# Performance work log

Measured on AMD Instinct MI355X. Metric: run time of the kernel, lower is better.

Reference implementation:

```python
import jax, jax.numpy as jnp
import numpy as np


def setup_inputs() -> dict:
    key = jax.random.key(0)
    k1, k2, k3, k4 = jax.random.split(key, 4)
    B, T, C, H = 8, 2048, 1024, 64
    x = jax.random.normal(k1, (B, T, C), dtype=jnp.float32)
    Wq = jax.random.normal(k2, (C, H), dtype=jnp.float32) * (C ** -0.5)
    Wk = jax.random.normal(k3, (C, H), dtype=jnp.float32) * (C ** -0.5)
    Wv = jax.random.normal(k4, (C, H), dtype=jnp.float32) * (C ** -0.5)
    return {"x": x, "Wq": Wq, "Wk": Wk, "Wv": Wv}


def reference(x, Wq, Wk, Wv):
    # x: [B,T,C]; Wq/Wk/Wv: [C,H] (nn.Linear bias=False => x @ W)
    B, T, C = x.shape
    H = Wq.shape[-1]
    q = jnp.einsum('btc,ch->bth', x, Wq)
    k = jnp.einsum('btc,ch->bth', x, Wk)
    v = jnp.einsum('btc,ch->bth', x, Wv)
    scale = H ** -0.5
    att = jnp.einsum('bqh,bkh->bqk', q, k) * scale  # [B,T,T]
    causal = jnp.tril(jnp.ones((T, T), dtype=bool))
    att = jnp.where(causal, att, -jnp.inf)
    att = jax.nn.softmax(att, axis=-1)
    out = jnp.einsum('bqk,bkh->bqh', att, v)  # [B,T,H]
    return out
```

## Files before the change

### kernel.cpp

```cpp
#include <hip/hip_runtime.h>
#include <hip/hip_bf16.h>
#include <math.h>

#define BB 8
#define TT 2048
#define CC 1024
#define HH 64
#define BT (BB * TT)

typedef __attribute__((ext_vector_type(8))) short short8;
typedef __attribute__((ext_vector_type(4))) float floatx4;

static __device__ inline ushort f2bf(float f) {
    __hip_bfloat16 h = __float2bfloat16(f);
    return *reinterpret_cast<ushort*>(&h);
}
static __device__ inline unsigned int f2bf2(float lo, float hi) {
    __hip_bfloat162 h = __float22bfloat162_rn(make_float2(lo, hi));
    return *reinterpret_cast<unsigned int*>(&h);
}
static __device__ inline float bf2f(ushort u) {
    union { unsigned int i; float f; } c;
    c.i = ((unsigned int)u) << 16;
    return c.f;
}
static __device__ inline void gl_ldsf(const float* g, float* l) {
    __builtin_amdgcn_global_load_lds(
        (const __attribute__((address_space(1))) unsigned int*)g,
        (__attribute__((address_space(3))) unsigned int*)l,
        16, 0, 0);
}

__global__ __launch_bounds__(256) void wprep_kernel(
    const float* __restrict__ Wq, const float* __restrict__ Wk,
    const float* __restrict__ Wv, ushort* __restrict__ WbT)
{
    __shared__ float ws_[64 * 65];
    const int m  = blockIdx.x >> 4;
    const int kb = (blockIdx.x & 15) * 64;
    const float* W = (m == 0) ? Wq : (m == 1) ? Wk : Wv;
    const int t  = threadIdx.x;
    const int lr = t >> 4, lc = (t & 15) * 4;
    #pragma unroll
    for (int i = 0; i < 4; ++i) {
        const int row = lr + i * 16;
        float4 v = *(const float4*)&W[(size_t)(kb + row) * HH + lc];
        ws_[row * 65 + lc + 0] = v.x; ws_[row * 65 + lc + 1] = v.y;
        ws_[row * 65 + lc + 2] = v.z; ws_[row * 65 + lc + 3] = v.w;
    }
    __syncthreads();
    const int n = t & 63, kseg = t >> 6;
    union { ushort s[16]; uint4 q[2]; } u;
    #pragma unroll
    for (int j = 0; j < 16; ++j)
        u.s[j] = f2bf(ws_[(kseg * 16 + j) * 65 + n]);
    ushort* dst = &WbT[(size_t)(m * 64 + n) * 1024 + kb + kseg * 16];
    *(uint4*)&dst[0] = u.q[0];
    *(uint4*)&dst[8] = u.q[1];
}

__global__ __launch_bounds__(256) void qkv_kernel(
    const float* __restrict__ x, const ushort* __restrict__ WbT,
    ushort* __restrict__ qb, ushort* __restrict__ kbS, ushort* __restrict__ vS)
{
    __shared__ __align__(16) float Xs[4][2048];

    const int row0 = blockIdx.x * 32;
    const int t    = threadIdx.x;
    const int w    = t >> 6;
    const int lane = t & 63;
    const int l16  = lane & 15;
    const int quad = lane >> 4;
    const int ct0  = w * 3;

    const int d0 = lane & 1, d1 = (lane >> 1) & 1, d2 = (lane >> 2) & 1, d3 = (lane >> 3) & 1;
    const int quads = (d1 ^ d2 ^ d3) + 2 * (d2 ^ d3);
    const int hh    = d0 ^ d1 ^ d2 ^ d3;
    const int kof   = (w >> 1) * 32 + quads * 8 + hh * 4;
    const int rowA  = (w & 1) * 16 + ((lane >> 3) & 7);
    const float* srcA = &x[(size_t)(row0 + rowA) * CC + kof];
    const float* srcB = srcA + (size_t)8 * CC;

    int off[4][2];
    #pragma unroll
    for (int f = 0; f < 4; ++f) {
        const int Sr = f * 64 + l16 * 4 + quad;
        const int sw = (Sr & 7) << 4;
        off[f][0] = (Sr * 32) ^ sw;
        off[f][1] = (Sr * 32 + 16) ^ sw;
    }

    floatx4 acc[2][3];
    #pragma unroll
    for (int mt = 0; mt < 2; ++mt)
        #pragma unroll
        for (int c = 0; c < 3; ++c) acc[mt][c] = (floatx4){0.f, 0.f, 0.f, 0.f};

    #define STAGE(buf, itx) do {                                   \
        gl_ldsf(srcA + (itx) * 64, &Xs[buf][w * 512]);             \
        gl_ldsf(srcB + (itx) * 64, &Xs[buf][w * 512 + 256]);       \
    } while (0)

    STAGE(0, 0); STAGE(1, 1); STAGE(2, 2);
    asm volatile("" ::: "memory");

    short8 bW[2][2][3];
    #pragma unroll
    for (int s = 0; s < 2; ++s)
        #pragma unroll
        for (int p = 0; p < 2; ++p)
            #pragma unroll
            for (int c = 0; c < 3; ++c)
                bW[s][p][c] = *(const short8*)&WbT[(size_t)((ct0 + c) * 16 + l16) * 1024
                                                   + s * 64 + p * 32 + quad * 8];

    #pragma unroll
    for (int it = 0; it < 16; ++it) {
        if (it == 0)       asm volatile("s_waitcnt vmcnt(16)" ::: "memory");
        else if (it < 14)  asm volatile("s_waitcnt vmcnt(22)" ::: "memory");
        else if (it == 14) asm volatile("s_waitcnt vmcnt(20)" ::: "memory");
        else               asm volatile("s_waitcnt vmcnt(12)" ::: "memory");
        __builtin_amdgcn_s_barrier();

        if (it + 3 < 16) STAGE((it + 3) & 3, it + 3);
        asm volatile("" ::: "memory");

        const char* bufc = (const char*)&Xs[it & 3][0];
        short8 a[4];
        #pragma unroll
        for (int f = 0; f < 4; ++f) {
            float4 lo = *(const float4*)(bufc + off[f][0]);
            float4 hi = *(const float4*)(bufc + off[f][1]);
            union { unsigned int u[4]; short8 s; } cv;
            cv.u[0] = f2bf2(lo.x, lo.y); cv.u[1] = f2bf2(lo.z, lo.w);
            cv.u[2] = f2bf2(hi.x, hi.y); cv.u[3] = f2bf2(hi.z, hi.w);
            a[f] = cv.s;
        }

        __builtin_amdgcn_s_setprio(1);
        #pragma unroll
        for (int c = 0; c < 3; ++c) {
            acc[0][c] = __builtin_amdgcn_mfma_f32_16x16x32_bf16(a[0], bW[it & 1][0][c], acc[0][c], 0, 0, 0);
            acc[1][c] = __builtin_amdgcn_mfma_f32_16x16x32_bf16(a[1], bW[it & 1][0][c], acc[1][c], 0, 0, 0);
            acc[0][c] = __builtin_amdgcn_mfma_f32_16x16x32_bf16(a[2], bW[it & 1][1][c], acc[0][c], 0, 0, 0);
            acc[1][c] = __builtin_amdgcn_mfma_f32_16x16x32_bf16(a[3], bW[it & 1][1][c], acc[1][c], 0, 0, 0);
        }
        __builtin_amdgcn_s_setprio(0);

        if (it + 2 < 16) {
            const int kn = (it + 2) * 64;
            #pragma unroll
            for (int p = 0; p < 2; ++p)
                #pragma unroll
                for (int c = 0; c < 3; ++c)
                    bW[it & 1][p][c] = *(const short8*)&WbT[(size_t)((ct0 + c) * 16 + l16) * 1024
                                                            + kn + p * 32 + quad * 8];
        }
    }
    #undef STAGE

    const int half = (row0 >> 5) & 1;
    const size_t tile = (size_t)(row0 >> 6) * 4096;
    #pragma unroll
    for (int c = 0; c < 3; ++c) {
        const int ct    = ct0 + c;
        const int mtype = ct >> 2;
        const int n0    = (ct & 3) * 16;
        #pragma unroll
        for (int mt = 0; mt < 2; ++mt) {
            const int row = row0 + mt * 16 + quad * 4;
            if (mtype == 0) {
                #pragma unroll
                for (int reg = 0; reg < 4; ++reg)
                    qb[(size_t)(row + reg) * HH + n0 + l16] = f2bf(acc[mt][c][reg] * 0.125f);
            } else if (mtype == 1) {
                const int cP    = half * 2 + mt;
                const int pP    = (ct & 3) >> 1;
                const int quadP = ((ct & 3) * 2 + (l16 >> 3)) & 3;
                const int jP    = l16 & 7;
                const int ub    = (cP * 2 + pP) * 64 + quadP * 16;
                #pragma unroll
                for (int reg = 0; reg < 4; ++reg)
                    kbS[tile + (size_t)(ub + quad * 4 + reg) * 8 + jP] = f2bf(acc[mt][c][reg]);
            } else {
                const int cp2 = (ct & 3) * 2 + half;
                #pragma unroll
                for (int reg = 0; reg < 4; ++reg) {
                    const int rq    = quad * 4 + reg;
                    const int quadP = mt * 2 + (rq >> 3);
                    vS[tile + (size_t)(cp2 * 64 + quadP * 16 + l16) * 8 + (rq & 7)] = f2bf(acc[mt][c][reg]);
                }
            }
        }
    }
}

__global__ __launch_bounds__(256) void attn_kernel(
    const ushort* __restrict__ qb, const ushort* __restrict__ kbS,
    const ushort* __restrict__ vS, ushort* __restrict__ Opart,
    float* __restrict__ ml)
{
    __shared__ __align__(16) ushort P[4][16 * 72];

    const int t    = threadIdx.x;
    const int w    = t >> 6;
    const int lane = t & 63;
    const int l16  = lane & 15;
    const int quad = lane >> 4;

    const int b   = blockIdx.x & 7;
    const int idx = blockIdx.x >> 3;
    int qt, part, np;
    if (idx < 32)      { qt = 31 - (idx >> 2); part = idx & 3; np = 4; }
    else if (idx < 56) { const int u = idx - 32; const int g = u / 3;
                         qt = 23 - g; part = u - g * 3; np = 3; }
    else if (idx < 72) { const int u = idx - 56; qt = 15 - (u >> 1); part = u & 1; np = 2; }
    else               { qt = 7 - (idx - 72); part = 0; np = 1; }
    const int ntiles = qt + 1;
    const int ktb = (part * ntiles) / np;
    const int kte = ((part + 1) * ntiles) / np;

    const ushort* ktile0 = kbS + (size_t)(b * 32) * 4096;
    const ushort* vtile0 = vS  + (size_t)(b * 32) * 4096;

    short8 qf[2];
    {
        const ushort* qrow = qb + ((size_t)b * TT + qt * 64 + w * 16) * HH;
        qf[0] = *(const short8*)&qrow[l16 * HH + quad * 8];
        qf[1] = *(const short8*)&qrow[l16 * HH + 32 + quad * 8];
    }
    short8 ones;
    #pragma unroll
    for (int i = 0; i < 8; ++i) ones[i] = (short)0x3F80;

    floatx4 o[4], osum;
    #pragma unroll
    for (int c = 0; c < 4; ++c) o[c] = (floatx4){0.f, 0.f, 0.f, 0.f};
    osum = (floatx4){0.f, 0.f, 0.f, 0.f};

    ushort* Pw = &P[w][0];

    for (int kt = ktb; kt < kte; ++kt) {
        const ushort* kg = ktile0 + (size_t)kt * 4096;
        const ushort* vg = vtile0 + (size_t)kt * 4096;

        short8 kf[4][2];
        #pragma unroll
        for (int c = 0; c < 4; ++c)
            #pragma unroll
            for (int p = 0; p < 2; ++p)
                kf[c][p] = *(const short8*)&kg[(size_t)(((c * 2 + p) * 64) + lane) * 8];

        floatx4 s[4];
        #pragma unroll
        for (int c = 0; c < 4; ++c) s[c] = (floatx4){0.f, 0.f, 0.f, 0.f};
        __builtin_amdgcn_s_setprio(1);
        #pragma unroll
        for (int c = 0; c < 4; ++c)
            #pragma unroll
            for (int p = 0; p < 2; ++p)
                s[c] = __builtin_amdgcn_mfma_f32_16x16x32_bf16(kf[c][p], qf[p], s[c], 0, 0, 0);
        __builtin_amdgcn_s_setprio(0);

        short8 vf[4][2];
        #pragma unroll
        for (int c = 0; c < 4; ++c)
            #pragma unroll
            for (int p = 0; p < 2; ++p)
                vf[c][p] = *(const short8*)&vg[(size_t)(((c * 2 + p) * 64) + lane) * 8];

        if (kt == ntiles - 1) {
            const int key0 = kt * 64 + quad * 4;
            const int qrow = qt * 64 + w * 16 + l16;
            #pragma unroll
            for (int c = 0; c < 4; ++c)
                #pragma unroll
                for (int reg = 0; reg < 4; ++reg)
                    if (key0 + c * 16 + reg > qrow) s[c][reg] = -1e30f;
        }

        #pragma unroll
        for (int c = 0; c < 4; ++c) {
            uint2 u;
            u.x = f2bf2(__expf(s[c][0]), __expf(s[c][1]));
            u.y = f2bf2(__expf(s[c][2]), __expf(s[c][3]));
            *(uint2*)&Pw[l16 * 72 + c * 16 + quad * 4] = u;
        }

        short8 pf[2];
        pf[0] = *(const short8*)&Pw[l16 * 72 + quad * 8];
        pf[1] = *(const short8*)&Pw[l16 * 72 + 32 + quad * 8];

        __builtin_amdgcn_s_setprio(1);
        #pragma unroll
        for (int p = 0; p < 2; ++p) {
            #pragma unroll
            for (int c = 0; c < 4; ++c)
                o[c] = __builtin_amdgcn_mfma_f32_16x16x32_bf16(pf[p], vf[c][p], o[c], 0, 0, 0);
            osum = __builtin_amdgcn_mfma_f32_16x16x32_bf16(pf[p], ones, osum, 0, 0, 0);
        }
        __builtin_amdgcn_s_setprio(0);
    }

    const size_t ub = (size_t)blockIdx.x * 4096;
    const int rbase = w * 16 + quad * 4;
    #pragma unroll
    for (int c = 0; c < 4; ++c) {
        uint2 u;
        u.x = f2bf2(o[c][0], o[c][1]);
        u.y = f2bf2(o[c][2], o[c][3]);
        *(uint2*)&Opart[ub + (size_t)(c * 16 + l16) * 64 + rbase] = u;
    }
    if (l16 == 0) {
        #pragma unroll
        for (int reg = 0; reg < 4; ++reg)
            ml[(size_t)blockIdx.x * 64 + rbase + reg] = osum[reg];
    }
}

__global__ __launch_bounds__(256) void merge_kernel(
    const ushort* __restrict__ Opart, const float* __restrict__ ml,
    float* __restrict__ out)
{
    const int t    = threadIdx.x;
    const int gw   = blockIdx.x * 4 + (t >> 6);
    const int lane = t & 63;
    const int b    = gw >> 8;
    const int v    = gw & 255;
    const int qt   = v >> 3;
    const int oct  = v & 7;

    int base, np;
    if (qt >= 24)      { base = (31 - qt) * 4;      np = 4; }
    else if (qt >= 16) { base = 32 + (23 - qt) * 3; np = 3; }
    else if (qt >= 8)  { base = 56 + (15 - qt) * 2; np = 2; }
    else               { base = 72 + (7 - qt);      np = 1; }

    float* obase = out + ((size_t)b * TT + qt * 64) * HH;

    #pragma unroll
    for (int rg = 0; rg < 2; ++rg) {
        const int row0 = oct * 8 + rg * 4;
        float dx = 0.f, dy = 0.f, dz = 0.f, dw = 0.f;
        float ax = 0.f, ay = 0.f, az = 0.f, aw = 0.f;
        for (int p = 0; p < np; ++p) {
            const int unit = (base + p) * 8 + b;
            float4 d = *(const float4*)&ml[(size_t)unit * 64 + row0];
            dx += d.x; dy += d.y; dz += d.z; dw += d.w;
            ushort4 ov = *(const ushort4*)&Opart[(size_t)unit * 4096 + lane * 64 + row0];
            ax += bf2f(ov.x); ay += bf2f(ov.y); az += bf2f(ov.z); aw += bf2f(ov.w);
        }
        obase[(size_t)(row0 + 0) * HH + lane] = ax / dx;
        obase[(size_t)(row0 + 1) * HH + lane] = ay / dy;
        obase[(size_t)(row0 + 2) * HH + lane] = az / dz;
        obase[(size_t)(row0 + 3) * HH + lane] = aw / dw;
    }
}

extern "C" void kernel_launch(void* const* d_in, const int* in_sizes, int n_in,
                              void* d_out, int out_size, void* d_ws, size_t ws_size,
                              hipStream_t stream)
{
    (void)in_sizes; (void)n_in; (void)out_size; (void)ws_size;
    const float* x  = (const float*)d_in[0];
    const float* Wq = (const float*)d_in[1];
    const float* Wk = (const float*)d_in[2];
    const float* Wv = (const float*)d_in[3];
    float* outp = (float*)d_out;

    char* base = (char*)d_ws;
    ushort* WbT   = (ushort*)(base);
    ushort* qbuf  = (ushort*)(base + 393216);
    ushort* kbS   = qbuf + (size_t)BT * HH;
    ushort* vSb   = kbS + (size_t)BT * HH;
    ushort* Opart = vSb + (size_t)BT * HH;
    float*  ml    = (float*)((char*)Opart + (size_t)640 * 4096 * 2);

    wprep_kernel<<<dim3(48),  256, 0, stream>>>(Wq, Wk, Wv, WbT);
    qkv_kernel  <<<dim3(512), 256, 0, stream>>>(x, WbT, qbuf, kbS, vSb);
    attn_kernel <<<dim3(640), 256, 0, stream>>>(qbuf, kbS, vSb, Opart, ml);
    merge_kernel<<<dim3(512), 256, 0, stream>>>(Opart, ml, outp);
}
```

Before: 136.0 us.

## Split QKV projection across output column groups to triple grid size

The QKV kernel now launches 1536 blocks instead of 512. Each block handles 32 rows and one group of four 16-column tiles (one per wave), rather than all twelve column tiles across four waves. The X staging buffer shrinks from four stages to three, with a prefetch depth of two, and launch bounds request six blocks per CU. This is meant to raise parallelism and occupancy, at the cost of each X tile being loaded from global memory three times and converted to bf16 three times.

```diff
diff --git a/kernel.cpp b/kernel.cpp
--- a/kernel.cpp
+++ b/kernel.cpp
@@ -59,19 +59,21 @@
     *(uint4*)&dst[8] = u.q[1];
 }
 
-__global__ __launch_bounds__(256) void qkv_kernel(
+__global__ __launch_bounds__(256, 6) void qkv_kernel(
     const float* __restrict__ x, const ushort* __restrict__ WbT,
     ushort* __restrict__ qb, ushort* __restrict__ kbS, ushort* __restrict__ vS)
 {
-    __shared__ __align__(16) float Xs[4][2048];
-
-    const int row0 = blockIdx.x * 32;
+    __shared__ __align__(16) float Xs[3][2048];
+
     const int t    = threadIdx.x;
     const int w    = t >> 6;
     const int lane = t & 63;
     const int l16  = lane & 15;
     const int quad = lane >> 4;
-    const int ct0  = w * 3;
+
+    const int bid  = blockIdx.x;
+    const int row0 = (bid & 511) * 32;
+    const int ct   = (bid >> 9) * 4 + w;
 
     const int d0 = lane & 1, d1 = (lane >> 1) & 1, d2 = (lane >> 2) & 1, d3 = (lane >> 3) & 1;
     const int quads = (d1 ^ d2 ^ d3) + 2 * (d2 ^ d3);
@@ -90,42 +92,40 @@
         off[f][1] = (Sr * 32 + 16) ^ sw;
     }
 
-    floatx4 acc[2][3];
-    #pragma unroll
-    for (int mt = 0; mt < 2; ++mt)
-        #pragma unroll
-        for (int c = 0; c < 3; ++c) acc[mt][c] = (floatx4){0.f, 0.f, 0.f, 0.f};
+    floatx4 acc[2];
+    acc[0] = (floatx4){0.f, 0.f, 0.f, 0.f};
+    acc[1] = (floatx4){0.f, 0.f, 0.f, 0.f};
 
     #define STAGE(buf, itx) do {                                   \
         gl_ldsf(srcA + (itx) * 64, &Xs[buf][w * 512]);             \
         gl_ldsf(srcB + (itx) * 64, &Xs[buf][w * 512 + 256]);       \
     } while (0)
 
-    STAGE(0, 0); STAGE(1, 1); STAGE(2, 2);
+    STAGE(0, 0); STAGE(1, 1);
     asm volatile("" ::: "memory");
 
-    short8 bW[2][2][3];
+    const ushort* wbase = &WbT[(size_t)(ct * 16 + l16) * 1024 + quad * 8];
+    short8 bW[2][2];
     #pragma unroll
     for (int s = 0; s < 2; ++s)
         #pragma unroll
         for (int p = 0; p < 2; ++p)
-            #pragma unroll
-            for (int c = 0; c < 3; ++c)
-                bW[s][p][c] = *(const short8*)&WbT[(size_t)((ct0 + c) * 16 + l16) * 1024
-                                                   + s * 64 + p * 32 + quad * 8];
-
+            bW[s][p] = *(const short8*)&wbase[s * 64 + p * 32];
+
+    int cur = 0;
     #pragma unroll
     for (int it = 0; it < 16; ++it) {
-        if (it == 0)       asm volatile("s_waitcnt vmcnt(16)" ::: "memory");
-        else if (it < 14)  asm volatile("s_waitcnt vmcnt(22)" ::: "memory");
-        else if (it == 14) asm volatile("s_waitcnt vmcnt(20)" ::: "memory");
-        else               asm volatile("s_waitcnt vmcnt(12)" ::: "memory");
+        if (it < 15) asm volatile("s_waitcnt vmcnt(6)" ::: "memory");
+        else         asm volatile("s_waitcnt vmcnt(2)" ::: "memory");
         __builtin_amdgcn_s_barrier();
 
-        if (it + 3 < 16) STAGE((it + 3) & 3, it + 3);
+        if (it + 2 < 16) {
+            int nb = cur + 2; if (nb >= 3) nb -= 3;
+            STAGE(nb, it + 2);
+        }
         asm volatile("" ::: "memory");
 
-        const char* bufc = (const char*)&Xs[it & 3][0];
+        const char* bufc = (const char*)&Xs[cur][0];
         short8 a[4];
         #pragma unroll
         for (int f = 0; f < 4; ++f) {
@@ -138,58 +138,49 @@
         }
 
         __builtin_amdgcn_s_setprio(1);
-        #pragma unroll
-        for (int c = 0; c < 3; ++c) {
-            acc[0][c] = __builtin_amdgcn_mfma_f32_16x16x32_bf16(a[0], bW[it & 1][0][c], acc[0][c], 0, 0, 0);
-            acc[1][c] = __builtin_amdgcn_mfma_f32_16x16x32_bf16(a[1], bW[it & 1][0][c], acc[1][c], 0, 0, 0);
-            acc[0][c] = __builtin_amdgcn_mfma_f32_16x16x32_bf16(a[2], bW[it & 1][1][c], acc[0][c], 0, 0, 0);
-            acc[1][c] = __builtin_amdgcn_mfma_f32_16x16x32_bf16(a[3], bW[it & 1][1][c], acc[1][c], 0, 0, 0);
-        }
+        acc[0] = __builtin_amdgcn_mfma_f32_16x16x32_bf16(a[0], bW[it & 1][0], acc[0], 0, 0, 0);
+        acc[1] = __builtin_amdgcn_mfma_f32_16x16x32_bf16(a[1], bW[it & 1][0], acc[1], 0, 0, 0);
+        acc[0] = __builtin_amdgcn_mfma_f32_16x16x32_bf16(a[2], bW[it & 1][1], acc[0], 0, 0, 0);
+        acc[1] = __builtin_amdgcn_mfma_f32_16x16x32_bf16(a[3], bW[it & 1][1], acc[1], 0, 0, 0);
         __builtin_amdgcn_s_setprio(0);
 
         if (it + 2 < 16) {
             const int kn = (it + 2) * 64;
             #pragma unroll
             for (int p = 0; p < 2; ++p)
-                #pragma unroll
-                for (int c = 0; c < 3; ++c)
-                    bW[it & 1][p][c] = *(const short8*)&WbT[(size_t)((ct0 + c) * 16 + l16) * 1024
-                                                            + kn + p * 32 + quad * 8];
-        }
+                bW[it & 1][p] = *(const short8*)&wbase[kn + p * 32];
+        }
+        cur = (cur + 1 < 3) ? cur + 1 : 0;
     }
     #undef STAGE
 
-    const int half = (row0 >> 5) & 1;
+    const int mtype = ct >> 2;
+    const int n0    = (ct & 3) * 16;
+    const int half  = (row0 >> 5) & 1;
     const size_t tile = (size_t)(row0 >> 6) * 4096;
     #pragma unroll
-    for (int c = 0; c < 3; ++c) {
-        const int ct    = ct0 + c;
-        const int mtype = ct >> 2;
-        const int n0    = (ct & 3) * 16;
-        #pragma unroll
-        for (int mt = 0; mt < 2; ++mt) {
-            const int row = row0 + mt * 16 + quad * 4;
-            if (mtype == 0) {
-                #pragma unroll
-                for (int reg = 0; reg < 4; ++reg)
-                    qb[(size_t)(row + reg) * HH + n0 + l16] = f2bf(acc[mt][c][reg] * 0.125f);
-            } else if (mtype == 1) {
-                const int cP    = half * 2 + mt;
-                const int pP    = (ct & 3) >> 1;
-                const int quadP = ((ct & 3) * 2 + (l16 >> 3)) & 3;
-                const int jP    = l16 & 7;
-                const int ub    = (cP * 2 + pP) * 64 + quadP * 16;
-                #pragma unroll
-                for (int reg = 0; reg < 4; ++reg)
-                    kbS[tile + (size_t)(ub + quad * 4 + reg) * 8 + jP] = f2bf(acc[mt][c][reg]);
-            } else {
-                const int cp2 = (ct & 3) * 2 + half;
-                #pragma unroll
-                for (int reg = 0; reg < 4; ++reg) {
-                    const int rq    = quad * 4 + reg;
-                    const int quadP = mt * 2 + (rq >> 3);
-                    vS[tile + (size_t)(cp2 * 64 + quadP * 16 + l16) * 8 + (rq & 7)] = f2bf(acc[mt][c][reg]);
-                }
+    for (int mt = 0; mt < 2; ++mt) {
+        const int row = row0 + mt * 16 + quad * 4;
+        if (mtype == 0) {
+            #pragma unroll
+            for (int reg = 0; reg < 4; ++reg)
+                qb[(size_t)(row + reg) * HH + n0 + l16] = f2bf(acc[mt][reg] * 0.125f);
+        } else if (mtype == 1) {
+            const int cP    = half * 2 + mt;
+            const int pP    = (ct & 3) >> 1;
+            const int quadP = ((ct & 3) * 2 + (l16 >> 3)) & 3;
+            const int jP    = l16 & 7;
+            const int ub    = (cP * 2 + pP) * 64 + quadP * 16;
+            #pragma unroll
+            for (int reg = 0; reg < 4; ++reg)
+                kbS[tile + (size_t)(ub + quad * 4 + reg) * 8 + jP] = f2bf(acc[mt][reg]);
+        } else {
+            const int cp2 = (ct & 3) * 2 + half;
+            #pragma unroll
+            for (int reg = 0; reg < 4; ++reg) {
+                const int rq    = quad * 4 + reg;
+                const int quadP = mt * 2 + (rq >> 3);
+                vS[tile + (size_t)(cp2 * 64 + quadP * 16 + l16) * 8 + (rq & 7)] = f2bf(acc[mt][reg]);
             }
         }
     }
@@ -376,8 +367,8 @@
     ushort* Opart = vSb + (size_t)BT * HH;
     float*  ml    = (float*)((char*)Opart + (size_t)640 * 4096 * 2);
 
-    wprep_kernel<<<dim3(48),  256, 0, stream>>>(Wq, Wk, Wv, WbT);
-    qkv_kernel  <<<dim3(512), 256, 0, stream>>>(x, WbT, qbuf, kbS, vSb);
-    attn_kernel <<<dim3(640), 256, 0, stream>>>(qbuf, kbS, vSb, Opart, ml);
-    merge_kernel<<<dim3(512), 256, 0, stream>>>(Opart, ml, outp);
-}
+    wprep_kernel<<<dim3(48),   256, 0, stream>>>(Wq, Wk, Wv, WbT);
+    qkv_kernel  <<<dim3(1536), 256, 0, stream>>>(x, WbT, qbuf, kbS, vSb);
+    attn_kernel <<<dim3(640),  256, 0, stream>>>(qbuf, kbS, vSb, Opart, ml);
+    merge_kernel<<<dim3(512),  256, 0, stream>>>(Opart, ml, outp);
+}
```

Result: slower. 147.5 us (+8.5%).
